# Performance work log

Measured on AMD Instinct MI355X. Metric: run time of the kernel, lower is better.

## Reference

```python
import jax, jax.numpy as jnp
import numpy as np

N_NODES = 25000
N_EDGES = 300000
N_GRAPHS = 256
EMB_DIM = 92
HID = 256
EDGE_F = 4


def _lin(key, fan_in, fan_out):
    kw, kb = jax.random.split(key)
    s = 1.0 / np.sqrt(fan_in)
    W = jax.random.uniform(kw, (fan_in, fan_out), jnp.float32, -s, s)
    b = jax.random.uniform(kb, (fan_out,), jnp.float32, -s, s)
    return W, b


def setup_inputs() -> dict:
    key = jax.random.key(0)
    ks = jax.random.split(key, 32)
    x_atoms = jax.random.randint(ks[0], (N_NODES,), 0, 119)
    edge_index = jax.random.randint(ks[1], (2, N_EDGES), 0, N_NODES)
    edge_attr = jax.random.normal(ks[2], (N_EDGES, EDGE_F), jnp.float32)
    batch = jnp.sort(jax.random.randint(ks[3], (N_NODES,), 0, N_GRAPHS))
    emb = jax.random.normal(ks[4], (119, EMB_DIM), jnp.float32)
    emb = emb.at[0].set(0.0)  # padding_idx=0
    # layer 0: in=92, out=256
    ew1_0, eb1_0 = _lin(ks[5], EDGE_F, EMB_DIM)
    ew2_0, eb2_0 = _lin(ks[6], EMB_DIM, EMB_DIM)
    nw_0, nb_0 = _lin(ks[7], EMB_DIM, HID)
    # layers 1..3 stacked: in=out=256
    ew1, eb1, ew2, eb2, nw, nb = [], [], [], [], [], []
    for i in range(3):
        a, b = _lin(ks[8 + 3 * i], EDGE_F, HID)
        c, d = _lin(ks[9 + 3 * i], HID, HID)
        e, f = _lin(ks[10 + 3 * i], HID, HID)
        ew1.append(a); eb1.append(b); ew2.append(c); eb2.append(d); nw.append(e); nb.append(f)
    ew1 = jnp.stack(ew1); eb1 = jnp.stack(eb1); ew2 = jnp.stack(ew2)
    eb2 = jnp.stack(eb2); nw = jnp.stack(nw); nb = jnp.stack(nb)
    rw1, rb1 = _lin(ks[20], HID, HID)
    rw2, rb2 = _lin(ks[21], HID, HID // 2)
    rw3, rb3 = _lin(ks[22], HID // 2, 1)
    return dict(x_atoms=x_atoms, edge_index=edge_index, edge_attr=edge_attr, batch=batch,
                emb=emb, ew1_0=ew1_0, eb1_0=eb1_0, ew2_0=ew2_0, eb2_0=eb2_0, nw_0=nw_0, nb_0=nb_0,
                ew1=ew1, eb1=eb1, ew2=ew2, eb2=eb2, nw=nw, nb=nb,
                rw1=rw1, rb1=rb1, rw2=rw2, rb2=rb2, rw3=rw3, rb3=rb3)


def _conv(x, src, dst, edge_attr, ew1, eb1, ew2, eb2, nw, nb):
    # edge MLP: Linear -> Softplus -> Linear
    ee = jax.nn.softplus(edge_attr @ ew1 + eb1) @ ew2 + eb2  # [E, C]
    msg = ee * x[src]                                        # gather + multiply
    agg = jax.ops.segment_sum(msg, dst, num_segments=x.shape[0])  # scatter-add
    return jax.nn.softplus(agg @ nw + nb)


def reference(x_atoms, edge_index, edge_attr, batch, emb,
              ew1_0, eb1_0, ew2_0, eb2_0, nw_0, nb_0,
              ew1, eb1, ew2, eb2, nw, nb,
              rw1, rb1, rw2, rb2, rw3, rb3):
    src, dst = edge_index[0], edge_index[1]  # PyG: x_j = x[src], aggregate at dst
    x = emb[x_atoms]  # [N, 92]
    x = _conv(x, src, dst, edge_attr, ew1_0, eb1_0, ew2_0, eb2_0, nw_0, nb_0)
    for i in range(3):
        x = _conv(x, src, dst, edge_attr, ew1[i], eb1[i], ew2[i], eb2[i], nw[i], nb[i])
    # global mean pool
    sums = jax.ops.segment_sum(x, batch, num_segments=N_GRAPHS)
    cnts = jax.ops.segment_sum(jnp.ones((x.shape[0],), x.dtype), batch, num_segments=N_GRAPHS)
    g = sums / jnp.maximum(cnts, 1.0)[:, None]  # [G, 256]
    h = jax.nn.softplus(g @ rw1 + rb1)          # dropout is identity in eval mode
    h = jax.nn.softplus(h @ rw2 + rb2)
    out = (h @ rw3 + rb3).squeeze(-1)           # [G]
    return out
```

## Files before the change

### kernel.cpp

```cpp
#include <hip/hip_runtime.h>
#include <math.h>

#define N_NODES  25000
#define N_EDGES  300000
#define N_GRAPHS 256
#define EMB_DIM  92
#define HID      256

typedef short bf16x8 __attribute__((ext_vector_type(8)));
typedef float f32x4  __attribute__((ext_vector_type(4)));

__device__ __forceinline__ float softplusf(float x){
    const float u = __expf(-fabsf(x));
    const float p = u*fmaf(u, fmaf(u, fmaf(u, fmaf(u, 0.03215845f, -0.13606275f),
                                            0.28947478f), -0.49190896f), 0.99949556f);
    return fmaxf(x, 0.0f) + p;
}
__device__ __forceinline__ unsigned short f2bf(float f){
    unsigned int u = __float_as_uint(f);
    unsigned int r = (u + 0x7FFFu + ((u >> 16) & 1u)) >> 16;
    return (unsigned short)r;
}
__device__ __forceinline__ unsigned short f2bf_trunc(float f){
    return (unsigned short)(__float_as_uint(f) >> 16);
}
__device__ __forceinline__ float bf2f(unsigned short b){
    return __uint_as_float(((unsigned int)b) << 16);
}
__device__ __forceinline__ void split_bf(float h, unsigned short& hi, unsigned short& lo){
    const unsigned int u = __float_as_uint(h);
    hi = (unsigned short)(u >> 16);
    const float r = h - __uint_as_float(u & 0xFFFF0000u);
    lo = (unsigned short)(__float_as_uint(r) >> 16);
}
__device__ __forceinline__ int xcd_window(int nwin){
    const int per = (nwin + 7) >> 3;
    const int win = (blockIdx.x & 7) * per + (blockIdx.x >> 3);
    return (win < nwin) ? win : -1;
}

__global__ void gather_emb_kernel(const int* __restrict__ atoms,
                                  const float* __restrict__ emb,
                                  float* __restrict__ x,
                                  int* __restrict__ hist, int* __restrict__ gcnt,
                                  float* __restrict__ sums)
{
    const int n = blockIdx.x;
    const int c = threadIdx.x;
    const int flat = n*128 + c;
    if (flat < N_NODES) hist[flat] = 0;
    if (flat < N_GRAPHS) gcnt[flat] = 0;
    if (flat < N_GRAPHS*HID) sums[flat] = 0.0f;
    if (c < EMB_DIM){
        const int a = atoms[n];
        x[(size_t)n*EMB_DIM + c] = emb[(size_t)a*EMB_DIM + c];
    }
}

__global__ __launch_bounds__(256) void hist_kernel(const int* __restrict__ dst, int* __restrict__ hist,
                                                   const int* __restrict__ batch, int* __restrict__ gcnt){
    const int e = blockIdx.x*256 + threadIdx.x;
    if (e < N_EDGES) atomicAdd(&hist[dst[e]], 1);
    if (e < N_NODES) atomicAdd(&gcnt[batch[e]], 1);
}

__global__ __launch_bounds__(1024) void scan_kernel(const int* __restrict__ hist, int* __restrict__ cursor){
    __shared__ int chunk[1024];
    const int t = threadIdx.x;
    const int base = t*25;
    int local[25];
    int s = 0;
    #pragma unroll
    for (int i=0;i<25;i++){
        const int idx = base+i;
        const int v = (idx < N_NODES) ? hist[idx] : 0;
        local[i] = s; s += v;
    }
    chunk[t] = s;
    __syncthreads();
    for (int off=1; off<1024; off<<=1){
        int v = (t >= off) ? chunk[t-off] : 0;
        __syncthreads();
        chunk[t] += v;
        __syncthreads();
    }
    const int pre = (t > 0) ? chunk[t-1] : 0;
    #pragma unroll
    for (int i=0;i<25;i++){
        const int idx = base+i;
        if (idx < N_NODES) cursor[idx] = pre + local[i];
    }
}

__global__ __launch_bounds__(256) void scatter_kernel(const int* __restrict__ src, const int* __restrict__ dst,
                                                      const float* __restrict__ ea,
                                                      int* __restrict__ cursor,
                                                      int* __restrict__ src_s, int* __restrict__ dst_s,
                                                      float* __restrict__ ea_s,
                                                      float* __restrict__ agg92){
    const int e = blockIdx.x*256 + threadIdx.x;
    if (e < N_EDGES){
        const int d = dst[e];
        const int pos = atomicAdd(&cursor[d], 1);
        src_s[pos] = src[e];
        dst_s[pos] = d;
        const float4 a = *(const float4*)(ea + (size_t)e*4);
        *(float4*)(ea_s + (size_t)pos*4) = a;
    }
    const int nth = gridDim.x*256;
    for (int i = blockIdx.x*256 + threadIdx.x; i < N_NODES*EMB_DIM; i += nth)
        agg92[i] = 0.0f;
}

__device__ __forceinline__ void pack256_dev(const float* w, unsigned short* whi, unsigned short* wlo, int f){
    const int layer = f >> 7;
    const int rem   = f & 127;
    const int ntile = rem >> 3;
    const int k8    = rem & 7;
    for (int i = threadIdx.x; i < 512; i += 256){
        const int lane = i >> 3, j = i & 7;
        const int k = k8*32 + (lane >> 4)*8 + j;
        const int n = ntile*16 + (lane & 15);
        const float v = w[(size_t)layer*HID*HID + (size_t)k*HID + n];
        const unsigned short hb = f2bf(v);
        whi[(size_t)f*512 + i] = hb;
        wlo[(size_t)f*512 + i] = f2bf(v - bf2f(hb));
    }
}
__device__ __forceinline__ void packpad_dev(const float* w, int Kin, int Nin, int ldn,
                                            unsigned short* whi, unsigned short* wlo, int f){
    const int k8 = f % 3;
    const int ntile = f / 3;
    for (int i = threadIdx.x; i < 512; i += 256){
        const int lane = i >> 3, j = i & 7;
        const int k = k8*32 + (lane >> 4)*8 + j;
        const int n = ntile*16 + (lane & 15);
        float v = 0.0f;
        if (k < Kin && n < Nin) v = w[(size_t)k*ldn + n];
        const unsigned short hb = f2bf(v);
        whi[(size_t)f*512 + i] = hb;
        wlo[(size_t)f*512 + i] = f2bf(v - bf2f(hb));
    }
}
__global__ __launch_bounds__(256) void pack_all_kernel(
    const float* __restrict__ ew2, const float* __restrict__ nw,
    const float* __restrict__ ew2_0, const float* __restrict__ nw_0,
    unsigned short* whi, unsigned short* wlo,
    unsigned short* nwhi, unsigned short* nwlo,
    unsigned short* w92hi, unsigned short* w92lo,
    unsigned short* nw92hi, unsigned short* nw92lo)
{
    const int b = blockIdx.x;
    if (b < 384)      pack256_dev(ew2, whi, wlo, b);
    else if (b < 768) pack256_dev(nw, nwhi, nwlo, b-384);
    else if (b < 786) packpad_dev(ew2_0, EMB_DIM, EMB_DIM, EMB_DIM, w92hi, w92lo, b-768);
    else              packpad_dev(nw_0, EMB_DIM, HID, HID, nw92hi, nw92lo, b-786);
}

__global__ __launch_bounds__(256, 4) void edge_conv92_mfma_kernel(
    const int* __restrict__ src_s, const int* __restrict__ dst_s,
    const float* __restrict__ ea_s,
    const float* __restrict__ w1, const float* __restrict__ b1,
    const unsigned short* __restrict__ whi, const unsigned short* __restrict__ wlo,
    const float* __restrict__ b2,
    const float* __restrict__ x92, float* __restrict__ agg92)
{
    constexpr int C = EMB_DIM;
    constexpr int KP = 96;
    constexpr int LDA = 104;
    constexpr int EPB = 64;
    constexpr int NWIN = (N_EDGES + EPB - 1) / EPB;
    __shared__ unsigned short aHi[EPB][LDA];
    __shared__ float eaS[EPB][4];
    __shared__ int   srcS[EPB];
    __shared__ int   dstS[EPB];

    const int win = xcd_window(NWIN);
    if (win < 0) return;
    const int e0  = win * EPB;
    const int tid = threadIdx.x;

    {
        const int e = tid >> 2, comp = tid & 3;
        const int eid = min(e0 + e, N_EDGES-1);
        eaS[e][comp] = ea_s[(size_t)eid*4 + comp];
        if (tid < EPB){
            const int eid2 = min(e0 + tid, N_EDGES-1);
            srcS[tid] = src_s[eid2];
            dstS[tid] = dst_s[eid2];
        }
    }
    __syncthreads();

    for (int idx = tid; idx < EPB*KP; idx += 256){
        const int e = idx / KP, k = idx - e*KP;
        float h = 0.0f;
        if (k < C){
            const float4 a = *(const float4*)&eaS[e][0];
            h = softplusf(fmaf(a.x, w1[k], fmaf(a.y, w1[C+k],
                          fmaf(a.z, w1[2*C+k], fmaf(a.w, w1[3*C+k], b1[k])))));
        }
        const int row = (e>>5)*32 + ((e>>2)&1)*16 + ((e>>3)&3)*4 + (e&3);
        aHi[row][k] = f2bf_trunc(h);
    }
    __syncthreads();

    const int lane = tid & 63, wv = tid >> 6;
    const int quad = lane >> 4, fcol = lane & 15;
    const int mpair = wv >> 1;
    const int ngrp  = wv & 1;

    f32x4 acc[2][3];
    #pragma unroll
    for (int m=0;m<2;m++)
        #pragma unroll
        for (int t=0;t<3;t++)
            #pragma unroll
            for (int j=0;j<4;j++) acc[m][t][j] = 0.0f;

    for (int k8=0;k8<3;k8++){
        bf16x8 ah[2];
        #pragma unroll
        for (int m=0;m<2;m++)
            ah[m] = *(const bf16x8*)(&aHi[mpair*32 + m*16 + fcol][0] + k8*32 + quad*8);
        #pragma unroll
        for (int t=0;t<3;t++){
            const int fi = (ngrp*3 + t)*3 + k8;
            const bf16x8 bh = *(const bf16x8*)(whi + (size_t)fi*512 + lane*8);
            const bf16x8 bl = *(const bf16x8*)(wlo + (size_t)fi*512 + lane*8);
            #pragma unroll
            for (int m=0;m<2;m++){
                acc[m][t] = __builtin_amdgcn_mfma_f32_16x16x32_bf16(ah[m], bh, acc[m][t], 0, 0, 0);
                acc[m][t] = __builtin_amdgcn_mfma_f32_16x16x32_bf16(ah[m], bl, acc[m][t], 0, 0, 0);
            }
        }
    }

    int   ncol[3]; float bb[3];
    #pragma unroll
    for (int t=0;t<3;t++){
        ncol[t] = (ngrp*3 + t)*16 + fcol;
        bb[t] = (ncol[t] < C) ? b2[ncol[t]] : 0.0f;
    }

    const int ebase = mpair*32 + quad*8;
    float xv[8][3];
    #pragma unroll
    for (int j=0;j<8;j++){
        const int s = srcS[ebase + j];
        const bool valid = (e0 + ebase + j) < N_EDGES;
        #pragma unroll
        for (int t=0;t<3;t++)
            xv[j][t] = (valid && ncol[t] < C) ? x92[(size_t)s*C + ncol[t]] : 0.0f;
    }

    int dprev = dstS[ebase];
    float run[3] = {0.f,0.f,0.f};
    #pragma unroll
    for (int j=0;j<8;j++){
        const int d = dstS[ebase + j];
        if (d != dprev){
            #pragma unroll
            for (int t=0;t<3;t++){
                if (ncol[t] < C) atomicAdd(&agg92[(size_t)dprev*C + ncol[t]], run[t]);
                run[t] = 0.0f;
            }
            dprev = d;
        }
        #pragma unroll
        for (int t=0;t<3;t++)
            run[t] += (acc[j>>2][t][j&3] + bb[t]) * xv[j][t];
    }
    #pragma unroll
    for (int t=0;t<3;t++)
        if (ncol[t] < C) atomicAdd(&agg92[(size_t)dprev*C + ncol[t]], run[t]);
}

__global__ __launch_bounds__(256) void node_update92_mfma_kernel(
    float* __restrict__ agg92,
    float* __restrict__ aggfull,
    const unsigned short* __restrict__ whi, const unsigned short* __restrict__ wlo,
    const float* __restrict__ b, float* __restrict__ xout)
{
    constexpr int C = EMB_DIM;
    constexpr int KP = 96;
    constexpr int LDA = 104;
    __shared__ unsigned short aHi[16][LDA];
    __shared__ unsigned short aLo[16][LDA];

    const int n0  = blockIdx.x * 16;
    const int tid = threadIdx.x;

    for (int idx = tid; idx < 16*KP; idx += 256){
        const int i = idx / KP, k = idx - i*KP;
        const int node = n0 + i;
        float v = 0.0f;
        if (k < C && node < N_NODES){
            v = agg92[(size_t)node*C + k];
            agg92[(size_t)node*C + k] = 0.0f;
        }
        unsigned short hb, lb;
        split_bf(v, hb, lb);
        aHi[i][k] = hb;
        aLo[i][k] = lb;
    }
    __syncthreads();

    const int lane = tid & 63, wv = tid >> 6;
    const int quad = lane >> 4, fcol = lane & 15;

    f32x4 acc[4];
    #pragma unroll
    for (int t=0;t<4;t++)
        #pragma unroll
        for (int j=0;j<4;j++) acc[t][j] = 0.0f;

    const unsigned short* aHrow = &aHi[fcol][0];
    const unsigned short* aLrow = &aLo[fcol][0];

    for (int k8=0;k8<3;k8++){
        const bf16x8 ah = *(const bf16x8*)(aHrow + k8*32 + quad*8);
        const bf16x8 al = *(const bf16x8*)(aLrow + k8*32 + quad*8);
        #pragma unroll
        for (int t=0;t<4;t++){
            const int fi = (wv*4 + t)*3 + k8;
            const bf16x8 bh = *(const bf16x8*)(whi + (size_t)fi*512 + lane*8);
            const bf16x8 bl = *(const bf16x8*)(wlo + (size_t)fi*512 + lane*8);
            acc[t] = __builtin_amdgcn_mfma_f32_16x16x32_bf16(ah, bh, acc[t], 0, 0, 0);
            acc[t] = __builtin_amdgcn_mfma_f32_16x16x32_bf16(ah, bl, acc[t], 0, 0, 0);
            acc[t] = __builtin_amdgcn_mfma_f32_16x16x32_bf16(al, bh, acc[t], 0, 0, 0);
        }
    }

    #pragma unroll
    for (int i=0;i<4;i++){
        const int node = n0 + quad*4 + i;
        if (node < N_NODES){
            #pragma unroll
            for (int t=0;t<4;t++){
                const int n = (wv*4 + t)*16 + fcol;
                xout[(size_t)node*HID + n] = softplusf(acc[t][i] + b[n]);
            }
        }
    }

    const int nth = gridDim.x*256;
    for (int idx = blockIdx.x*256 + tid; idx < N_NODES*164; idx += nth)
        aggfull[idx] = 0.0f;
}

__global__ __launch_bounds__(512, 6) void edge_conv256_mfma_kernel(
    const int* __restrict__ src_s, const int* __restrict__ dst_s,
    const float* __restrict__ ea_s,
    const float* __restrict__ w1, const float* __restrict__ b1,
    const unsigned short* __restrict__ whi,
    const float* __restrict__ b2,
    const float* __restrict__ x, float* __restrict__ agg)
{
    constexpr int C = HID;
    constexpr int LDA = C + 8;
    constexpr int EPB = 64;
    constexpr int NWIN = (N_EDGES + EPB - 1) / EPB;
    __shared__ unsigned short aHi[EPB][LDA];
    __shared__ float eaS[EPB][4];
    __shared__ int   srcS[EPB];
    __shared__ int   dstS[EPB];

    const int win = xcd_window(NWIN);
    if (win < 0) return;
    const int e0  = win * EPB;
    const int tid = threadIdx.x;

    if (tid < 256){
        const int e = tid >> 2, comp = tid & 3;
        const int eid = min(e0 + e, N_EDGES-1);
        eaS[e][comp] = ea_s[(size_t)eid*4 + comp];
    } else if (tid < 320){
        const int e = tid - 256;
        srcS[e] = src_s[min(e0 + e, N_EDGES-1)];
    } else if (tid < 384){
        const int e = tid - 320;
        dstS[e] = dst_s[min(e0 + e, N_EDGES-1)];
    }
    __syncthreads();

    {
        const int k2 = (tid & 127) * 2;
        const int g  = tid >> 7;
        const float wa0 = w1[k2],   wa1 = w1[C+k2],   wa2 = w1[2*C+k2],   wa3 = w1[3*C+k2];
        const float wb0 = w1[k2+1], wb1 = w1[C+k2+1], wb2 = w1[2*C+k2+1], wb3 = w1[3*C+k2+1];
        const float bk0 = b1[k2], bk1 = b1[k2+1];
        #pragma unroll
        for (int ii=0; ii<16; ii++){
            const int e = g*16 + ii;
            const float4 a = *(const float4*)&eaS[e][0];
            const float v0 = fmaf(a.x,wa0,fmaf(a.y,wa1,fmaf(a.z,wa2,fmaf(a.w,wa3,bk0))));
            const float v1 = fmaf(a.x,wb0,fmaf(a.y,wb1,fmaf(a.z,wb2,fmaf(a.w,wb3,bk1))));
            const unsigned int packed = (unsigned int)f2bf_trunc(softplusf(v0))
                                      | ((unsigned int)f2bf_trunc(softplusf(v1)) << 16);
            const int q = e >> 4, j = e & 15;
            *(unsigned int*)&aHi[(j>>2)*16 + q*4 + (j&3)][k2] = packed;
        }
    }
    __syncthreads();

    const int lane = tid & 63, wv = tid >> 6;
    const int quad = lane >> 4, fcol = lane & 15;

    f32x4 acc[4][2];
    #pragma unroll
    for (int m=0;m<4;m++)
        #pragma unroll
        for (int t=0;t<2;t++)
            #pragma unroll
            for (int j=0;j<4;j++) acc[m][t][j] = 0.0f;

    for (int k8=0;k8<8;k8++){
        bf16x8 ah[4];
        #pragma unroll
        for (int m=0;m<4;m++)
            ah[m] = *(const bf16x8*)(&aHi[m*16 + fcol][0] + k8*32 + quad*8);
        #pragma unroll
        for (int t=0;t<2;t++){
            const int fi = (wv*2 + t)*8 + k8;
            const bf16x8 bh = *(const bf16x8*)(whi + (size_t)fi*512 + lane*8);
            #pragma unroll
            for (int m=0;m<4;m++)
                acc[m][t] = __builtin_amdgcn_mfma_f32_16x16x32_bf16(ah[m], bh, acc[m][t], 0, 0, 0);
        }
    }

    float bb[2];
    #pragma unroll
    for (int t=0;t<2;t++) bb[t] = b2[(wv*2 + t)*16 + fcol];

    const int ebase = quad*16;
    float xv[16][2];
    #pragma unroll
    for (int j=0;j<16;j++){
        const int s = srcS[ebase + j];
        const bool valid = (e0 + ebase + j) < N_EDGES;
        #pragma unroll
        for (int t=0;t<2;t++)
            xv[j][t] = valid ? x[(size_t)s*C + (wv*2 + t)*16 + fcol] : 0.0f;
    }

    int dprev = dstS[ebase];
    float run[2] = {0.f,0.f};
    #pragma unroll
    for (int j=0;j<16;j++){
        const int d = dstS[ebase + j];
        if (d != dprev){
            #pragma unroll
            for (int t=0;t<2;t++){
                atomicAdd(&agg[(size_t)dprev*C + (wv*2 + t)*16 + fcol], run[t]);
                run[t] = 0.0f;
            }
            dprev = d;
        }
        #pragma unroll
        for (int t=0;t<2;t++)
            run[t] += (acc[j>>2][t][j&3] + bb[t]) * xv[j][t];
    }
    #pragma unroll
    for (int t=0;t<2;t++)
        atomicAdd(&agg[(size_t)dprev*C + (wv*2 + t)*16 + fcol], run[t]);
}

__global__ __launch_bounds__(256) void node_update_mfma_kernel(
    float* __restrict__ agg,
    const unsigned short* __restrict__ whi, const unsigned short* __restrict__ wlo,
    const float* __restrict__ b, float* __restrict__ xout, int zero_agg,
    const int* __restrict__ batch, float* __restrict__ sums, int do_pool)
{
    constexpr int C = HID;
    constexpr int LDA = C + 8;
    __shared__ unsigned short aHi[16][LDA];
    __shared__ unsigned short aLo[16][LDA];
    __shared__ int batchS[16];

    const int n0  = blockIdx.x * 16;
    const int tid = threadIdx.x;

    if (tid < 16) batchS[tid] = batch[min(n0 + tid, N_NODES-1)];

    #pragma unroll
    for (int it=0; it<16; it++){
        const int node = n0 + it;
        float v = 0.0f;
        if (node < N_NODES){
            v = agg[(size_t)node*C + tid];
            if (zero_agg) agg[(size_t)node*C + tid] = 0.0f;
        }
        unsigned short hb, lb;
        split_bf(v, hb, lb);
        aHi[it][tid] = hb;
        aLo[it][tid] = lb;
    }
    __syncthreads();

    const int lane = tid & 63, wv = tid >> 6;
    const int quad = lane >> 4, fcol = lane & 15;

    f32x4 acc[4];
    #pragma unroll
    for (int t=0;t<4;t++)
        #pragma unroll
        for (int j=0;j<4;j++) acc[t][j] = 0.0f;

    const unsigned short* aHrow = &aHi[fcol][0];
    const unsigned short* aLrow = &aLo[fcol][0];

    for (int k8=0;k8<8;k8++){
        const bf16x8 ah = *(const bf16x8*)(aHrow + k8*32 + quad*8);
        const bf16x8 al = *(const bf16x8*)(aLrow + k8*32 + quad*8);
        #pragma unroll
        for (int t=0;t<4;t++){
            const int fi = (wv*4 + t)*8 + k8;
            const bf16x8 bh = *(const bf16x8*)(whi + (size_t)fi*512 + lane*8);
            const bf16x8 bl = *(const bf16x8*)(wlo + (size_t)fi*512 + lane*8);
            acc[t] = __builtin_amdgcn_mfma_f32_16x16x32_bf16(ah, bh, acc[t], 0, 0, 0);
            acc[t] = __builtin_amdgcn_mfma_f32_16x16x32_bf16(ah, bl, acc[t], 0, 0, 0);
            acc[t] = __builtin_amdgcn_mfma_f32_16x16x32_bf16(al, bh, acc[t], 0, 0, 0);
        }
    }

    float vals[4][4];
    #pragma unroll
    for (int i=0;i<4;i++){
        const int node = n0 + quad*4 + i;
        #pragma unroll
        for (int t=0;t<4;t++){
            float v = 0.0f;
            if (node < N_NODES){
                const int n = (wv*4 + t)*16 + fcol;
                v = softplusf(acc[t][i] + b[n]);
                xout[(size_t)node*C + n] = v;
            }
            vals[i][t] = v;
        }
    }

    if (do_pool){
        int gprev = batchS[quad*4];
        float run[4] = {0.f,0.f,0.f,0.f};
        #pragma unroll
        for (int i=0;i<4;i++){
            const int g = batchS[quad*4 + i];
            if (g != gprev){
                #pragma unroll
                for (int t=0;t<4;t++){
                    atomicAdd(&sums[(size_t)gprev*HID + (wv*4+t)*16 + fcol], run[t]);
                    run[t] = 0.0f;
                }
                gprev = g;
            }
            #pragma unroll
            for (int t=0;t<4;t++) run[t] += vals[i][t];
        }
        #pragma unroll
        for (int t=0;t<4;t++)
            atomicAdd(&sums[(size_t)gprev*HID + (wv*4+t)*16 + fcol], run[t]);
    }
}

__global__ __launch_bounds__(256) void readout_kernel(
    const float* __restrict__ sums, const int* __restrict__ gcnt,
    const float* __restrict__ rw1, const float* __restrict__ rb1,
    const float* __restrict__ rw2, const float* __restrict__ rb2,
    const float* __restrict__ rw3, const float* __restrict__ rb3,
    float* __restrict__ out)
{
    __shared__ float g[HID];
    __shared__ float h[HID];
    __shared__ float h2[HID/2];
    __shared__ float red[256];
    const int gi = blockIdx.x;
    const int t  = threadIdx.x;
    const float cnt = fmaxf((float)gcnt[gi], 1.0f);
    g[t] = sums[(size_t)gi*HID + t] / cnt;
    __syncthreads();
    float acc = rb1[t];
    for (int k=0;k<HID;k++) acc = fmaf(g[k], rw1[(size_t)k*HID + t], acc);
    h[t] = softplusf(acc);
    __syncthreads();
    if (t < HID/2){
        float a2 = rb2[t];
        for (int k=0;k<HID;k++) a2 = fmaf(h[k], rw2[(size_t)k*(HID/2) + t], a2);
        h2[t] = softplusf(a2);
    }
    __syncthreads();
    red[t] = (t < HID/2) ? h2[t]*rw3[t] : 0.0f;
    __syncthreads();
    for (int s2=128; s2>0; s2>>=1){
        if (t < s2) red[t] += red[t+s2];
        __syncthreads();
    }
    if (t == 0) out[gi] = red[0] + rb3[0];
}

extern "C" void kernel_launch(void* const* d_in, const int* in_sizes, int n_in,
                              void* d_out, int out_size, void* d_ws, size_t ws_size,
                              hipStream_t stream)
{
    const int*   x_atoms = (const int*)d_in[0];
    const int*   eidx    = (const int*)d_in[1];
    const int*   src     = eidx;
    const int*   dst     = eidx + N_EDGES;
    const float* ea      = (const float*)d_in[2];
    const int*   batch   = (const int*)d_in[3];
    const float* emb     = (const float*)d_in[4];
    const float* ew1_0   = (const float*)d_in[5];
    const float* eb1_0   = (const float*)d_in[6];
    const float* ew2_0   = (const float*)d_in[7];
    const float* eb2_0   = (const float*)d_in[8];
    const float* nw_0    = (const float*)d_in[9];
    const float* nb_0    = (const float*)d_in[10];
    const float* ew1     = (const float*)d_in[11];
    const float* eb1     = (const float*)d_in[12];
    const float* ew2     = (const float*)d_in[13];
    const float* eb2     = (const float*)d_in[14];
    const float* nw      = (const float*)d_in[15];
    const float* nb      = (const float*)d_in[16];
    const float* rw1     = (const float*)d_in[17];
    const float* rb1     = (const float*)d_in[18];
    const float* rw2     = (const float*)d_in[19];
    const float* rb2     = (const float*)d_in[20];
    const float* rw3     = (const float*)d_in[21];
    const float* rb3     = (const float*)d_in[22];
    float* out = (float*)d_out;

    float* x    = (float*)d_ws;
    float* agg  = x   + (size_t)N_NODES*HID;
    float* agg92 = agg + (size_t)N_NODES*164;
    float* sums = agg + (size_t)N_NODES*HID;
    unsigned short* whi  = (unsigned short*)(sums + (size_t)N_GRAPHS*HID);
    unsigned short* wlo  = whi  + (size_t)3*128*512;
    unsigned short* nwhi = wlo  + (size_t)3*128*512;
    unsigned short* nwlo = nwhi + (size_t)3*128*512;
    unsigned short* w92hi  = nwlo  + (size_t)3*128*512;
    unsigned short* w92lo  = w92hi + (size_t)18*512;
    unsigned short* nw92hi = w92lo + (size_t)18*512;
    unsigned short* nw92lo = nw92hi + (size_t)48*512;
    float* ea_s = (float*)(nw92lo + (size_t)48*512);
    int* hist   = (int*)(ea_s + (size_t)N_EDGES*4);
    int* gcnt   = hist   + N_NODES;
    int* cursor = gcnt   + N_GRAPHS;
    int* src_s  = cursor + N_NODES;
    int* dst_s  = src_s  + N_EDGES;

    const int NWIN64 = (N_EDGES + 63) / 64;

    hipLaunchKernelGGL(gather_emb_kernel, dim3(N_NODES), dim3(128), 0, stream,
                       x_atoms, emb, x, hist, gcnt, sums);
    hipLaunchKernelGGL(hist_kernel, dim3((N_EDGES+255)/256), dim3(256), 0, stream, dst, hist, batch, gcnt);
    hipLaunchKernelGGL(scan_kernel, dim3(1), dim3(1024), 0, stream, hist, cursor);
    hipLaunchKernelGGL(scatter_kernel, dim3((N_EDGES+255)/256), dim3(256), 0, stream,
                       src, dst, ea, cursor, src_s, dst_s, ea_s, agg92);
    hipLaunchKernelGGL(pack_all_kernel, dim3(834), dim3(256), 0, stream,
                       ew2, nw, ew2_0, nw_0,
                       whi, wlo, nwhi, nwlo, w92hi, w92lo, nw92hi, nw92lo);

    hipLaunchKernelGGL(edge_conv92_mfma_kernel, dim3((NWIN64+7)/8*8), dim3(256), 0, stream,
                       src_s, dst_s, ea_s, ew1_0, eb1_0, w92hi, w92lo, eb2_0, x, agg92);
    hipLaunchKernelGGL(node_update92_mfma_kernel, dim3((N_NODES+15)/16), dim3(256), 0, stream,
                       agg92, agg, nw92hi, nw92lo, nb_0, x);

    for (int i=0;i<3;i++){
        hipLaunchKernelGGL(edge_conv256_mfma_kernel, dim3((NWIN64+7)/8*8), dim3(512), 0, stream,
                           src_s, dst_s, ea_s,
                           ew1 + (size_t)i*4*HID, eb1 + (size_t)i*HID,
                           whi + (size_t)i*128*512,
                           eb2 + (size_t)i*HID,
                           x, agg);
        hipLaunchKernelGGL(node_update_mfma_kernel, dim3((N_NODES+15)/16), dim3(256), 0, stream,
                           agg, nwhi + (size_t)i*128*512, nwlo + (size_t)i*128*512,
                           nb + (size_t)i*HID, x, (i < 2) ? 1 : 0,
                           batch, sums, (i == 2) ? 1 : 0);
    }

    hipLaunchKernelGGL(readout_kernel, dim3(N_GRAPHS), dim3(256), 0, stream,
                       sums, gcnt, rw1, rb1, rw2, rb2, rw3, rb3, out);
}
```

Measured before the change: 648.2 us.

## Prefetch source gathers before edge MLP and drop lo-split for layer-0 weights

Both edge conv kernels now issue the x[src] gather loads before the edge-MLP softplus and MFMA phases, so gather latency can overlap compute. The 92-dim edge kernel drops the bf16 low-part weight correction, halving its MFMA count and weight loads at some precision cost. The 256-dim edge kernel's occupancy hint drops from 6 to 4 waves per SIMD to leave room for the extra live registers held by the prefetched values.

```diff
diff --git a/kernel.cpp b/kernel.cpp
--- a/kernel.cpp
+++ b/kernel.cpp
@@ -139,7 +139,7 @@
         if (k < Kin && n < Nin) v = w[(size_t)k*ldn + n];
         const unsigned short hb = f2bf(v);
         whi[(size_t)f*512 + i] = hb;
-        wlo[(size_t)f*512 + i] = f2bf(v - bf2f(hb));
+        if (wlo) wlo[(size_t)f*512 + i] = f2bf(v - bf2f(hb));
     }
 }
 __global__ __launch_bounds__(256) void pack_all_kernel(
@@ -147,13 +147,13 @@
     const float* __restrict__ ew2_0, const float* __restrict__ nw_0,
     unsigned short* whi, unsigned short* wlo,
     unsigned short* nwhi, unsigned short* nwlo,
-    unsigned short* w92hi, unsigned short* w92lo,
+    unsigned short* w92hi,
     unsigned short* nw92hi, unsigned short* nw92lo)
 {
     const int b = blockIdx.x;
     if (b < 384)      pack256_dev(ew2, whi, wlo, b);
     else if (b < 768) pack256_dev(nw, nwhi, nwlo, b-384);
-    else if (b < 786) packpad_dev(ew2_0, EMB_DIM, EMB_DIM, EMB_DIM, w92hi, w92lo, b-768);
+    else if (b < 786) packpad_dev(ew2_0, EMB_DIM, EMB_DIM, EMB_DIM, w92hi, (unsigned short*)0, b-768);
     else              packpad_dev(nw_0, EMB_DIM, HID, HID, nw92hi, nw92lo, b-786);
 }
 
@@ -161,7 +161,7 @@
     const int* __restrict__ src_s, const int* __restrict__ dst_s,
     const float* __restrict__ ea_s,
     const float* __restrict__ w1, const float* __restrict__ b1,
-    const unsigned short* __restrict__ whi, const unsigned short* __restrict__ wlo,
+    const unsigned short* __restrict__ whi,
     const float* __restrict__ b2,
     const float* __restrict__ x92, float* __restrict__ agg92)
 {
@@ -192,6 +192,24 @@
     }
     __syncthreads();
 
+    const int lane = tid & 63, wv = tid >> 6;
+    const int quad = lane >> 4, fcol = lane & 15;
+    const int mpair = wv >> 1;
+    const int ngrp  = wv & 1;
+    int ncol[3];
+    #pragma unroll
+    for (int t=0;t<3;t++) ncol[t] = (ngrp*3 + t)*16 + fcol;
+    const int ebase = mpair*32 + quad*8;
+    float xv[8][3];
+    #pragma unroll
+    for (int j=0;j<8;j++){
+        const int s = srcS[ebase + j];
+        const bool valid = (e0 + ebase + j) < N_EDGES;
+        #pragma unroll
+        for (int t=0;t<3;t++)
+            xv[j][t] = (valid && ncol[t] < C) ? x92[(size_t)s*C + ncol[t]] : 0.0f;
+    }
+
     for (int idx = tid; idx < EPB*KP; idx += 256){
         const int e = idx / KP, k = idx - e*KP;
         float h = 0.0f;
@@ -205,11 +223,6 @@
     }
     __syncthreads();
 
-    const int lane = tid & 63, wv = tid >> 6;
-    const int quad = lane >> 4, fcol = lane & 15;
-    const int mpair = wv >> 1;
-    const int ngrp  = wv & 1;
-
     f32x4 acc[2][3];
     #pragma unroll
     for (int m=0;m<2;m++)
@@ -227,32 +240,15 @@
         for (int t=0;t<3;t++){
             const int fi = (ngrp*3 + t)*3 + k8;
             const bf16x8 bh = *(const bf16x8*)(whi + (size_t)fi*512 + lane*8);
-            const bf16x8 bl = *(const bf16x8*)(wlo + (size_t)fi*512 + lane*8);
-            #pragma unroll
-            for (int m=0;m<2;m++){
+            #pragma unroll
+            for (int m=0;m<2;m++)
                 acc[m][t] = __builtin_amdgcn_mfma_f32_16x16x32_bf16(ah[m], bh, acc[m][t], 0, 0, 0);
-                acc[m][t] = __builtin_amdgcn_mfma_f32_16x16x32_bf16(ah[m], bl, acc[m][t], 0, 0, 0);
-            }
-        }
-    }
-
-    int   ncol[3]; float bb[3];
-    #pragma unroll
-    for (int t=0;t<3;t++){
-        ncol[t] = (ngrp*3 + t)*16 + fcol;
-        bb[t] = (ncol[t] < C) ? b2[ncol[t]] : 0.0f;
-    }
-
-    const int ebase = mpair*32 + quad*8;
-    float xv[8][3];
-    #pragma unroll
-    for (int j=0;j<8;j++){
-        const int s = srcS[ebase + j];
-        const bool valid = (e0 + ebase + j) < N_EDGES;
-        #pragma unroll
-        for (int t=0;t<3;t++)
-            xv[j][t] = (valid && ncol[t] < C) ? x92[(size_t)s*C + ncol[t]] : 0.0f;
-    }
+        }
+    }
+
+    float bb[3];
+    #pragma unroll
+    for (int t=0;t<3;t++) bb[t] = (ncol[t] < C) ? b2[ncol[t]] : 0.0f;
 
     int dprev = dstS[ebase];
     float run[3] = {0.f,0.f,0.f};
@@ -349,7 +345,7 @@
         aggfull[idx] = 0.0f;
 }
 
-__global__ __launch_bounds__(512, 6) void edge_conv256_mfma_kernel(
+__global__ __launch_bounds__(512, 4) void edge_conv256_mfma_kernel(
     const int* __restrict__ src_s, const int* __restrict__ dst_s,
     const float* __restrict__ ea_s,
     const float* __restrict__ w1, const float* __restrict__ b1,
@@ -384,6 +380,19 @@
     }
     __syncthreads();
 
+    const int lane = tid & 63, wv = tid >> 6;
+    const int quad = lane >> 4, fcol = lane & 15;
+    const int ebase = quad*16;
+    float xv[16][2];
+    #pragma unroll
+    for (int j=0;j<16;j++){
+        const int s = srcS[ebase + j];
+        const bool valid = (e0 + ebase + j) < N_EDGES;
+        #pragma unroll
+        for (int t=0;t<2;t++)
+            xv[j][t] = valid ? x[(size_t)s*C + (wv*2 + t)*16 + fcol] : 0.0f;
+    }
+
     {
         const int k2 = (tid & 127) * 2;
         const int g  = tid >> 7;
@@ -404,9 +413,6 @@
     }
     __syncthreads();
 
-    const int lane = tid & 63, wv = tid >> 6;
-    const int quad = lane >> 4, fcol = lane & 15;
-
     f32x4 acc[4][2];
     #pragma unroll
     for (int m=0;m<4;m++)
@@ -433,17 +439,6 @@
     float bb[2];
     #pragma unroll
     for (int t=0;t<2;t++) bb[t] = b2[(wv*2 + t)*16 + fcol];
-
-    const int ebase = quad*16;
-    float xv[16][2];
-    #pragma unroll
-    for (int j=0;j<16;j++){
-        const int s = srcS[ebase + j];
-        const bool valid = (e0 + ebase + j) < N_EDGES;
-        #pragma unroll
-        for (int t=0;t<2;t++)
-            xv[j][t] = valid ? x[(size_t)s*C + (wv*2 + t)*16 + fcol] : 0.0f;
-    }
 
     int dprev = dstS[ebase];
     float run[2] = {0.f,0.f};
@@ -639,8 +634,7 @@
     unsigned short* nwhi = wlo  + (size_t)3*128*512;
     unsigned short* nwlo = nwhi + (size_t)3*128*512;
     unsigned short* w92hi  = nwlo  + (size_t)3*128*512;
-    unsigned short* w92lo  = w92hi + (size_t)18*512;
-    unsigned short* nw92hi = w92lo + (size_t)18*512;
+    unsigned short* nw92hi = w92hi + (size_t)18*512;
     unsigned short* nw92lo = nw92hi + (size_t)48*512;
     float* ea_s = (float*)(nw92lo + (size_t)48*512);
     int* hist   = (int*)(ea_s + (size_t)N_EDGES*4);
@@ -659,10 +653,10 @@
                        src, dst, ea, cursor, src_s, dst_s, ea_s, agg92);
     hipLaunchKernelGGL(pack_all_kernel, dim3(834), dim3(256), 0, stream,
                        ew2, nw, ew2_0, nw_0,
-                       whi, wlo, nwhi, nwlo, w92hi, w92lo, nw92hi, nw92lo);
+                       whi, wlo, nwhi, nwlo, w92hi, nw92hi, nw92lo);
 
     hipLaunchKernelGGL(edge_conv92_mfma_kernel, dim3((NWIN64+7)/8*8), dim3(256), 0, stream,
-                       src_s, dst_s, ea_s, ew1_0, eb1_0, w92hi, w92lo, eb2_0, x, agg92);
+                       src_s, dst_s, ea_s, ew1_0, eb1_0, w92hi, eb2_0, x, agg92);
     hipLaunchKernelGGL(node_update92_mfma_kernel, dim3((N_NODES+15)/16), dim3(256), 0, stream,
                        agg92, agg, nw92hi, nw92lo, nb_0, x);
 
```

Result: slower. 698.5 us (+7.8%).
